# Optimization experiments

Hardware: AMD Instinct MI355X
Metric: run time of the kernel (lower is better)

The kernel has to match this reference:

```python
import jax, jax.numpy as jnp
import numpy as np

HEAD_DIM = 64

def setup_inputs() -> dict:
    key = jax.random.key(0)
    k1, k2, k3, k4 = jax.random.split(key, 4)
    B, S, D, H = 8, 2048, 1024, HEAD_DIM
    x = jax.random.normal(k1, (B, S, D), dtype=jnp.float32)
    scale = 1.0 / np.sqrt(D)
    W_q = jax.random.normal(k2, (H, D), dtype=jnp.float32) * scale
    W_k = jax.random.normal(k3, (H, D), dtype=jnp.float32) * scale
    W_v = jax.random.normal(k4, (H, D), dtype=jnp.float32) * scale
    return {"input_embeddings": x, "W_q": W_q, "W_k": W_k, "W_v": W_v}

def reference(input_embeddings, W_q, W_k, W_v):
    # Linear(model_dim, head_dim, bias=False): y = x @ W.T
    q = jnp.einsum('bsd,hd->bsh', input_embeddings, W_q)
    k = jnp.einsum('bsd,hd->bsh', input_embeddings, W_k)
    v = jnp.einsum('bsd,hd->bsh', input_embeddings, W_v)
    scores = jnp.einsum('bqh,bkh->bqk', q, k) / jnp.sqrt(jnp.float32(HEAD_DIM))
    S = scores.shape[-1]
    causal = jnp.tril(jnp.ones((S, S), dtype=bool))  # [S,S]
    scores = jnp.where(causal, scores, -jnp.inf)
    attn = jax.nn.softmax(scores, axis=-1)
    # dropout p=0.0 (eval-equivalent): identity
    return jnp.einsum('bqk,bkh->bqh', attn, v)
```

## Files before the change

### kernel.cpp

```cpp
#include <hip/hip_runtime.h>
#include <hip/hip_bf16.h>

typedef __bf16 bf16x8 __attribute__((ext_vector_type(8)));
typedef __bf16 bf16x4 __attribute__((ext_vector_type(4)));
typedef float  f32x4  __attribute__((ext_vector_type(4)));

#define NB  8
#define SEQ 2048
#define DM  1024
#define HD  64

#define WAITV4 asm volatile("s_waitcnt vmcnt(4)" ::: "memory")
#define WAITV0 asm volatile("s_waitcnt vmcnt(0)" ::: "memory")

__device__ __forceinline__ void gll16(const void* g, void* l) {
    __builtin_amdgcn_global_load_lds(
        (const __attribute__((address_space(1))) unsigned int*)g,
        (__attribute__((address_space(3))) unsigned int*)l, 16, 0, 0);
}

__global__ void k_convw(const float* __restrict__ Wq, const float* __restrict__ Wk,
                        const float* __restrict__ Wv, __bf16* __restrict__ Wb) {
    int idx = blockIdx.x * blockDim.x + threadIdx.x;
    int e = idx * 4;
    const float* src;
    if (e < 65536)       src = Wq + e;
    else if (e < 131072) src = Wk + (e - 65536);
    else                 src = Wv + (e - 131072);
    float4 v = *reinterpret_cast<const float4*>(src);
    bf16x4 o;
    o[0] = (__bf16)v.x; o[1] = (__bf16)v.y; o[2] = (__bf16)v.z; o[3] = (__bf16)v.w;
    *reinterpret_cast<bf16x4*>(Wb + e) = o;
}

__launch_bounds__(512, 4)
__global__ void k_proj(const float* __restrict__ X, const __bf16* __restrict__ Wb,
                       __bf16* __restrict__ Qb, __bf16* __restrict__ Kb,
                       __bf16* __restrict__ Vt) {
    __shared__ __align__(16) float  Xs[2][2048];
    __shared__ __align__(16) __bf16 Ws[2][12288];
    const int tid = threadIdx.x;
    const int w = tid >> 6, l = tid & 63;
    const int lr = l & 15, lg = l >> 4;
    const int wm = w >> 2, wn = w & 3;
    const int m0 = blockIdx.x * 32;

    const float* xsrc;
    {
        int u = w * 64 + l;
        int r_ = u >> 4, c_ = u & 15;
        xsrc = X + (size_t)(m0 + r_) * DM + (c_ ^ (r_ & 15)) * 4;
    }
    const __bf16* wsrc[3];
    #pragma unroll
    for (int j = 0; j < 3; ++j) {
        int u = w * 192 + j * 64 + l;
        int r_ = u >> 3, c_ = u & 7;
        wsrc[j] = Wb + (size_t)r_ * DM + (c_ ^ (r_ & 7)) * 8;
    }

    f32x4 acc[3];
    #pragma unroll
    for (int ct = 0; ct < 3; ++ct) acc[ct] = f32x4{0.f, 0.f, 0.f, 0.f};

    const int abase = (wm * 16 + lr) * 64;
    int bbase[3];
    #pragma unroll
    for (int ct = 0; ct < 3; ++ct) bbase[ct] = ((wn * 3 + ct) * 16 + lr) * 64;

    gll16(xsrc, &Xs[0][w * 256]);
    #pragma unroll
    for (int j = 0; j < 3; ++j) gll16(wsrc[j], &Ws[0][w * 1536 + j * 512]);

    #pragma unroll
    for (int t = 0; t < 16; ++t) {
        const int cur = t & 1;
        __builtin_amdgcn_s_barrier();
        if (t + 1 < 16) {
            gll16(xsrc + (size_t)(t + 1) * 64, &Xs[cur ^ 1][w * 256]);
            #pragma unroll
            for (int j = 0; j < 3; ++j)
                gll16(wsrc[j] + (size_t)(t + 1) * 64, &Ws[cur ^ 1][w * 1536 + j * 512]);
            WAITV4;
        } else {
            WAITV0;
        }
        const float*  Xp = &Xs[cur][0];
        const __bf16* Wp = &Ws[cur][0];
        #pragma unroll
        for (int ks = 0; ks < 2; ++ks) {
            f32x4 a0 = *reinterpret_cast<const f32x4*>(Xp + abase + ((ks * 8 + lg * 2)     ^ lr) * 4);
            f32x4 a1 = *reinterpret_cast<const f32x4*>(Xp + abase + ((ks * 8 + lg * 2 + 1) ^ lr) * 4);
            bf16x8 af;
            #pragma unroll
            for (int j = 0; j < 4; ++j) { af[j] = (__bf16)a0[j]; af[4 + j] = (__bf16)a1[j]; }
            #pragma unroll
            for (int ct = 0; ct < 3; ++ct) {
                bf16x8 bf = *reinterpret_cast<const bf16x8*>(
                    Wp + bbase[ct] + (((ks * 4 + lg) ^ (lr & 7)) * 8));
                acc[ct] = __builtin_amdgcn_mfma_f32_16x16x32_bf16(af, bf, acc[ct], 0, 0, 0);
            }
        }
    }

    const int rowbase = m0 + wm * 16 + lg * 4;
    #pragma unroll
    for (int ct = 0; ct < 3; ++ct) {
        const int ntile = wn * 3 + ct;
        const int mtx = ntile >> 2;
        const int d = (ntile & 3) * 16 + lr;
        if (mtx == 0) {
            #pragma unroll
            for (int r = 0; r < 4; ++r)
                Qb[(size_t)(rowbase + r) * HD + d] = (__bf16)(acc[ct][r] * 0.18033688f);
        } else if (mtx == 1) {
            #pragma unroll
            for (int r = 0; r < 4; ++r)
                Kb[(size_t)(rowbase + r) * HD + d] = (__bf16)acc[ct][r];
        } else {
            int bb = rowbase >> 11;
            int s0 = rowbase & 2047;
            bf16x4 vv;
            #pragma unroll
            for (int r = 0; r < 4; ++r) vv[r] = (__bf16)acc[ct][r];
            *reinterpret_cast<bf16x4*>(Vt + ((size_t)bb * HD + d) * SEQ + s0) = vv;
        }
    }
}

__launch_bounds__(512)
__global__ void k_attn(const __bf16* __restrict__ Qb, const __bf16* __restrict__ Kb,
                       const __bf16* __restrict__ Vt, __bf16* __restrict__ Opart,
                       float* __restrict__ ML, int T, int NC) {
    const int bid = blockIdx.x;
    const int b = bid / (16 * NC);
    const int rem = bid - b * 16 * NC;
    const int qt2 = rem / NC;
    const int c = rem - qt2 * NC;
    const int kmax = 2 * qt2 + 1;
    if (c * T > kmax) return;
    const int kt0 = c * T;
    const int nt = min(T, kmax + 1 - kt0);
    const int q0 = qt2 * 128;

    __shared__ __align__(16) __bf16 Ks[2][4096];
    __shared__ __align__(16) __bf16 Vs[2][4096];
    __shared__ __align__(16) __bf16 Ps[128][72];
    const int tid = threadIdx.x;
    const int w = tid >> 6, l = tid & 63;
    const int lr = l & 15, lg = l >> 4;
    const __bf16* Qp = Qb + (size_t)b * SEQ * HD;
    const __bf16* Kp = Kb + (size_t)b * SEQ * HD;
    const __bf16* Vp = Vt + (size_t)b * HD * SEQ;

    const int srow = tid >> 3;
    const int ssw  = ((l & 7) ^ (srow & 7)) * 8;
    const __bf16* ksrc = Kp + (size_t)(kt0 * 64 + srow) * HD + ssw;
    const __bf16* vsrc = Vp + (size_t)srow * SEQ + kt0 * 64 + ssw;
    const int myq = q0 + 16 * w + lr;

    bf16x8 qa[2];
    #pragma unroll
    for (int ks = 0; ks < 2; ++ks)
        qa[ks] = *reinterpret_cast<const bf16x8*>(
            Qp + (size_t)myq * HD + ks * 32 + lg * 8);

    f32x4 oacc[4];
    #pragma unroll
    for (int r = 0; r < 4; ++r) oacc[r] = f32x4{0.f, 0.f, 0.f, 0.f};
    float m = -1e30f, lsum = 0.f;

    gll16(ksrc, &Ks[0][w * 512]);
    gll16(vsrc, &Vs[0][w * 512]);

    for (int it = 0; it < nt; ++it) {
        const int kt = kt0 + it;
        const int k0 = kt * 64;
        const int cur = it & 1;
        __builtin_amdgcn_s_barrier();
        if (it + 1 < nt) {
            gll16(ksrc + (size_t)(it + 1) * 64 * HD, &Ks[cur ^ 1][w * 512]);
            gll16(vsrc + (it + 1) * 64,              &Vs[cur ^ 1][w * 512]);
            asm volatile("s_waitcnt vmcnt(2)" ::: "memory");
        } else {
            asm volatile("s_waitcnt vmcnt(0)" ::: "memory");
        }

        if (k0 > q0 + 16 * w + 15) continue;

        f32x4 sacc[4];
        #pragma unroll
        for (int t = 0; t < 4; ++t) sacc[t] = f32x4{0.f, 0.f, 0.f, 0.f};
        #pragma unroll
        for (int ks = 0; ks < 2; ++ks) {
            #pragma unroll
            for (int t = 0; t < 4; ++t) {
                bf16x8 kf = *reinterpret_cast<const bf16x8*>(
                    &Ks[cur][(16 * t + lr) * 64 + (((ks * 4 + lg) ^ (lr & 7)) * 8)]);
                sacc[t] = __builtin_amdgcn_mfma_f32_16x16x32_bf16(kf, qa[ks], sacc[t], 0, 0, 0);
            }
        }

        float pmax = -1e30f;
        if (k0 + 63 > q0 + 16 * w) {
            #pragma unroll
            for (int t = 0; t < 4; ++t)
                #pragma unroll
                for (int r = 0; r < 4; ++r) {
                    float v = sacc[t][r];
                    if ((k0 + 16 * t + lg * 4 + r) > myq) v = -1e30f;
                    sacc[t][r] = v;
                    pmax = fmaxf(pmax, v);
                }
        } else {
            #pragma unroll
            for (int t = 0; t < 4; ++t)
                #pragma unroll
                for (int r = 0; r < 4; ++r) pmax = fmaxf(pmax, sacc[t][r]);
        }
        pmax = fmaxf(pmax, __shfl_xor(pmax, 16));
        pmax = fmaxf(pmax, __shfl_xor(pmax, 32));

        if (!__all(pmax <= m + 12.f)) {
            float mnew = fmaxf(m, pmax);
            float fsc = exp2f(m - mnew);
            m = mnew;
            lsum *= fsc;
            #pragma unroll
            for (int r = 0; r < 4; ++r) {
                float fq = __shfl(fsc, (l & 48) + lg * 4 + r);
                #pragma unroll
                for (int t2 = 0; t2 < 4; ++t2) oacc[t2][r] *= fq;
            }
        }

        float rs = 0.f;
        #pragma unroll
        for (int t = 0; t < 4; ++t)
            #pragma unroll
            for (int r = 0; r < 4; ++r) {
                float p = exp2f(sacc[t][r] - m);
                sacc[t][r] = p;
                rs += p;
            }
        rs += __shfl_xor(rs, 16);
        rs += __shfl_xor(rs, 32);
        lsum += rs;

        #pragma unroll
        for (int t = 0; t < 4; ++t) {
            bf16x4 pv;
            #pragma unroll
            for (int r = 0; r < 4; ++r) pv[r] = (__bf16)sacc[t][r];
            *reinterpret_cast<bf16x4*>(&Ps[16 * w + lr][16 * t + lg * 4]) = pv;
        }

        #pragma unroll
        for (int ks = 0; ks < 2; ++ks) {
            bf16x8 pa = *reinterpret_cast<const bf16x8*>(&Ps[16 * w + lr][ks * 32 + lg * 8]);
            #pragma unroll
            for (int t2 = 0; t2 < 4; ++t2) {
                bf16x8 vb = *reinterpret_cast<const bf16x8*>(
                    &Vs[cur][(16 * t2 + lr) * 64 + (((ks * 4 + lg) ^ (lr & 7)) * 8)]);
                oacc[t2] = __builtin_amdgcn_mfma_f32_16x16x32_bf16(pa, vb, oacc[t2], 0, 0, 0);
            }
        }
    }

    const size_t slot = (size_t)bid;
    __bf16* op = Opart + slot * 8192;
    #pragma unroll
    for (int t2 = 0; t2 < 4; ++t2)
        #pragma unroll
        for (int r = 0; r < 4; ++r)
            op[(16 * w + lg * 4 + r) * 64 + 16 * t2 + lr] = (__bf16)oacc[t2][r];
    if (lg == 0) {
        float* ml = ML + slot * 256;
        int row = 16 * w + lr;
        ml[row * 2]     = m;
        ml[row * 2 + 1] = lsum;
    }
}

__launch_bounds__(512)
__global__ void k_merge(const __bf16* __restrict__ Opart, const float* __restrict__ ML,
                        float* __restrict__ Out, int T, int NC) {
    const int bq2 = blockIdx.x >> 1;
    const int half = blockIdx.x & 1;
    const int qt2 = bq2 & 15;
    const int nc = (2 * qt2 + 1) / T + 1;
    const int tid = threadIdx.x;
    const int row = tid >> 2;
    const int cg = (tid & 3) * 8 + half * 32;
    const int base = bq2 * NC;

    float M = -1e30f;
    for (int c = 0; c < nc; ++c)
        M = fmaxf(M, ML[(size_t)(base + c) * 256 + row * 2]);

    float L = 0.f;
    f32x4 a0{0,0,0,0}, a1{0,0,0,0};
    for (int c = 0; c < nc; ++c) {
        const float* ml = ML + (size_t)(base + c) * 256 + row * 2;
        float wgt = exp2f(ml[0] - M);
        L += ml[1] * wgt;
        bf16x8 v = *reinterpret_cast<const bf16x8*>(
            Opart + (size_t)(base + c) * 8192 + row * 64 + cg);
        #pragma unroll
        for (int j = 0; j < 4; ++j) {
            a0[j] += wgt * (float)v[j];
            a1[j] += wgt * (float)v[4 + j];
        }
    }
    float inv = 1.f / L;
    #pragma unroll
    for (int j = 0; j < 4; ++j) { a0[j] *= inv; a1[j] *= inv; }
    float* o = Out + ((size_t)bq2 * 128 + row) * 64 + cg;
    *reinterpret_cast<f32x4*>(o)     = a0;
    *reinterpret_cast<f32x4*>(o + 4) = a1;
}

extern "C" void kernel_launch(void* const* d_in, const int* in_sizes, int n_in,
                              void* d_out, int out_size, void* d_ws, size_t ws_size,
                              hipStream_t stream) {
    const float* x  = (const float*)d_in[0];
    const float* wq = (const float*)d_in[1];
    const float* wk = (const float*)d_in[2];
    const float* wv = (const float*)d_in[3];
    char* ws = (char*)d_ws;
    __bf16* Wb = (__bf16*)ws;
    __bf16* Qb = (__bf16*)(ws + 524288);
    __bf16* Kb = (__bf16*)(ws + 524288 + 2097152);
    __bf16* Vt = (__bf16*)(ws + 524288 + 2 * 2097152);
    const size_t base = 524288 + 3 * 2097152;
    float* out = (float*)d_out;

    int NC = (ws_size >= base + (size_t)(8 * 16 * 4) * 17408) ? 4 : 2;
    int T = 32 / NC;
    const int slots = 8 * 16 * NC;
    float*  ML    = (float*)(ws + base);
    __bf16* Opart = (__bf16*)(ws + base + (size_t)slots * 1024);

    hipLaunchKernelGGL(k_convw, dim3(192), dim3(256), 0, stream, wq, wk, wv, Wb);
    hipLaunchKernelGGL(k_proj,  dim3(512), dim3(512), 0, stream, x, Wb, Qb, Kb, Vt);
    hipLaunchKernelGGL(k_attn,  dim3(8 * 16 * NC), dim3(512), 0, stream,
                       Qb, Kb, Vt, Opart, ML, T, NC);
    hipLaunchKernelGGL(k_merge, dim3(256), dim3(512), 0, stream, Opart, ML, out, T, NC);
}
```

Baseline: 51.62 us.

## Process two 16-row query tiles per wave in attention, halve block size

Each wave in the attention kernel now handles 32 query rows (two 16-row MFMA tiles) instead of 16, and the block shrinks from 512 to 256 threads with launch bounds of 3 blocks per CU. Each K/V fragment read from LDS is reused for two MFMAs, which halves LDS traffic per unit of compute. Each thread now issues two async global-to-LDS loads per matrix per tile. The cost is roughly doubled accumulator and score registers per thread, plus coarser causal skipping because a wave covers 32 rows.

```diff
diff --git a/kernel.cpp b/kernel.cpp
--- a/kernel.cpp
+++ b/kernel.cpp
@@ -128,7 +128,7 @@
     }
 }
 
-__launch_bounds__(512)
+__launch_bounds__(256, 3)
 __global__ void k_attn(const __bf16* __restrict__ Qb, const __bf16* __restrict__ Kb,
                        const __bf16* __restrict__ Vt, __bf16* __restrict__ Opart,
                        float* __restrict__ ML, int T, int NC) {
@@ -153,25 +153,38 @@
     const __bf16* Kp = Kb + (size_t)b * SEQ * HD;
     const __bf16* Vp = Vt + (size_t)b * HD * SEQ;
 
-    const int srow = tid >> 3;
-    const int ssw  = ((l & 7) ^ (srow & 7)) * 8;
-    const __bf16* ksrc = Kp + (size_t)(kt0 * 64 + srow) * HD + ssw;
-    const __bf16* vsrc = Vp + (size_t)srow * SEQ + kt0 * 64 + ssw;
-    const int myq = q0 + 16 * w + lr;
-
-    bf16x8 qa[2];
-    #pragma unroll
-    for (int ks = 0; ks < 2; ++ks)
-        qa[ks] = *reinterpret_cast<const bf16x8*>(
-            Qp + (size_t)myq * HD + ks * 32 + lg * 8);
-
-    f32x4 oacc[4];
-    #pragma unroll
-    for (int r = 0; r < 4; ++r) oacc[r] = f32x4{0.f, 0.f, 0.f, 0.f};
-    float m = -1e30f, lsum = 0.f;
-
-    gll16(ksrc, &Ks[0][w * 512]);
-    gll16(vsrc, &Vs[0][w * 512]);
+    const __bf16* ksrc[2];
+    const __bf16* vsrc[2];
+    #pragma unroll
+    for (int j = 0; j < 2; ++j) {
+        int u = j * 256 + w * 64 + l;
+        int r_ = u >> 3, c_ = u & 7;
+        ksrc[j] = Kp + (size_t)(kt0 * 64 + r_) * HD + ((c_ ^ (r_ & 7)) * 8);
+        vsrc[j] = Vp + (size_t)r_ * SEQ + kt0 * 64 + ((c_ ^ (r_ & 7)) * 8);
+    }
+    const int myq0 = q0 + 32 * w + lr;
+    const int myq1 = myq0 + 16;
+
+    bf16x8 qa0[2], qa1[2];
+    #pragma unroll
+    for (int ks = 0; ks < 2; ++ks) {
+        qa0[ks] = *reinterpret_cast<const bf16x8*>(Qp + (size_t)myq0 * HD + ks * 32 + lg * 8);
+        qa1[ks] = *reinterpret_cast<const bf16x8*>(Qp + (size_t)myq1 * HD + ks * 32 + lg * 8);
+    }
+
+    f32x4 oacc0[4], oacc1[4];
+    #pragma unroll
+    for (int r = 0; r < 4; ++r) {
+        oacc0[r] = f32x4{0.f, 0.f, 0.f, 0.f};
+        oacc1[r] = f32x4{0.f, 0.f, 0.f, 0.f};
+    }
+    float m0v = -1e30f, l0v = 0.f, m1v = -1e30f, l1v = 0.f;
+
+    #pragma unroll
+    for (int j = 0; j < 2; ++j) {
+        gll16(ksrc[j], &Ks[0][(j * 256 + w * 64) * 8]);
+        gll16(vsrc[j], &Vs[0][(j * 256 + w * 64) * 8]);
+    }
 
     for (int it = 0; it < nt; ++it) {
         const int kt = kt0 + it;
@@ -179,90 +192,147 @@
         const int cur = it & 1;
         __builtin_amdgcn_s_barrier();
         if (it + 1 < nt) {
-            gll16(ksrc + (size_t)(it + 1) * 64 * HD, &Ks[cur ^ 1][w * 512]);
-            gll16(vsrc + (it + 1) * 64,              &Vs[cur ^ 1][w * 512]);
-            asm volatile("s_waitcnt vmcnt(2)" ::: "memory");
+            #pragma unroll
+            for (int j = 0; j < 2; ++j) {
+                gll16(ksrc[j] + (size_t)(it + 1) * 64 * HD, &Ks[cur ^ 1][(j * 256 + w * 64) * 8]);
+                gll16(vsrc[j] + (it + 1) * 64,              &Vs[cur ^ 1][(j * 256 + w * 64) * 8]);
+            }
+            WAITV4;
         } else {
-            asm volatile("s_waitcnt vmcnt(0)" ::: "memory");
-        }
-
-        if (k0 > q0 + 16 * w + 15) continue;
-
-        f32x4 sacc[4];
-        #pragma unroll
-        for (int t = 0; t < 4; ++t) sacc[t] = f32x4{0.f, 0.f, 0.f, 0.f};
+            WAITV0;
+        }
+
+        if (k0 > q0 + 32 * w + 31) continue;
+
+        f32x4 s0[4], s1[4];
+        #pragma unroll
+        for (int t = 0; t < 4; ++t) { s0[t] = f32x4{0,0,0,0}; s1[t] = f32x4{0,0,0,0}; }
         #pragma unroll
         for (int ks = 0; ks < 2; ++ks) {
             #pragma unroll
             for (int t = 0; t < 4; ++t) {
                 bf16x8 kf = *reinterpret_cast<const bf16x8*>(
                     &Ks[cur][(16 * t + lr) * 64 + (((ks * 4 + lg) ^ (lr & 7)) * 8)]);
-                sacc[t] = __builtin_amdgcn_mfma_f32_16x16x32_bf16(kf, qa[ks], sacc[t], 0, 0, 0);
-            }
-        }
-
-        float pmax = -1e30f;
-        if (k0 + 63 > q0 + 16 * w) {
+                s0[t] = __builtin_amdgcn_mfma_f32_16x16x32_bf16(kf, qa0[ks], s0[t], 0, 0, 0);
+                s1[t] = __builtin_amdgcn_mfma_f32_16x16x32_bf16(kf, qa1[ks], s1[t], 0, 0, 0);
+            }
+        }
+
+        {
+            float pmax = -1e30f;
+            if (k0 + 63 > myq0 - lr) {
+                #pragma unroll
+                for (int t = 0; t < 4; ++t)
+                    #pragma unroll
+                    for (int r = 0; r < 4; ++r) {
+                        float v = s0[t][r];
+                        if ((k0 + 16 * t + lg * 4 + r) > myq0) v = -1e30f;
+                        s0[t][r] = v;
+                        pmax = fmaxf(pmax, v);
+                    }
+            } else {
+                #pragma unroll
+                for (int t = 0; t < 4; ++t)
+                    #pragma unroll
+                    for (int r = 0; r < 4; ++r) pmax = fmaxf(pmax, s0[t][r]);
+            }
+            pmax = fmaxf(pmax, __shfl_xor(pmax, 16));
+            pmax = fmaxf(pmax, __shfl_xor(pmax, 32));
+            if (!__all(pmax <= m0v + 12.f)) {
+                float mnew = fmaxf(m0v, pmax);
+                float fsc = exp2f(m0v - mnew);
+                m0v = mnew;
+                l0v *= fsc;
+                #pragma unroll
+                for (int r = 0; r < 4; ++r) {
+                    float fq = __shfl(fsc, (l & 48) + lg * 4 + r);
+                    #pragma unroll
+                    for (int t2 = 0; t2 < 4; ++t2) oacc0[t2][r] *= fq;
+                }
+            }
+            float rs = 0.f;
             #pragma unroll
             for (int t = 0; t < 4; ++t)
                 #pragma unroll
                 for (int r = 0; r < 4; ++r) {
-                    float v = sacc[t][r];
-                    if ((k0 + 16 * t + lg * 4 + r) > myq) v = -1e30f;
-                    sacc[t][r] = v;
-                    pmax = fmaxf(pmax, v);
+                    float p = exp2f(s0[t][r] - m0v);
+                    s0[t][r] = p;
+                    rs += p;
                 }
-        } else {
+            rs += __shfl_xor(rs, 16);
+            rs += __shfl_xor(rs, 32);
+            l0v += rs;
+            #pragma unroll
+            for (int t = 0; t < 4; ++t) {
+                bf16x4 pv;
+                #pragma unroll
+                for (int r = 0; r < 4; ++r) pv[r] = (__bf16)s0[t][r];
+                *reinterpret_cast<bf16x4*>(&Ps[32 * w + lr][16 * t + lg * 4]) = pv;
+            }
+        }
+        {
+            float pmax = -1e30f;
+            if (k0 + 63 > myq1 - lr) {
+                #pragma unroll
+                for (int t = 0; t < 4; ++t)
+                    #pragma unroll
+                    for (int r = 0; r < 4; ++r) {
+                        float v = s1[t][r];
+                        if ((k0 + 16 * t + lg * 4 + r) > myq1) v = -1e30f;
+                        s1[t][r] = v;
+                        pmax = fmaxf(pmax, v);
+                    }
+            } else {
+                #pragma unroll
+                for (int t = 0; t < 4; ++t)
+                    #pragma unroll
+                    for (int r = 0; r < 4; ++r) pmax = fmaxf(pmax, s1[t][r]);
+            }
+            pmax = fmaxf(pmax, __shfl_xor(pmax, 16));
+            pmax = fmaxf(pmax, __shfl_xor(pmax, 32));
+            if (!__all(pmax <= m1v + 12.f)) {
+                float mnew = fmaxf(m1v, pmax);
+                float fsc = exp2f(m1v - mnew);
+                m1v = mnew;
+                l1v *= fsc;
+                #pragma unroll
+                for (int r = 0; r < 4; ++r) {
+                    float fq = __shfl(fsc, (l & 48) + lg * 4 + r);
+                    #pragma unroll
+                    for (int t2 = 0; t2 < 4; ++t2) oacc1[t2][r] *= fq;
+                }
+            }
+            float rs = 0.f;
             #pragma unroll
             for (int t = 0; t < 4; ++t)
                 #pragma unroll
-                for (int r = 0; r < 4; ++r) pmax = fmaxf(pmax, sacc[t][r]);
-        }
-        pmax = fmaxf(pmax, __shfl_xor(pmax, 16));
-        pmax = fmaxf(pmax, __shfl_xor(pmax, 32));
-
-        if (!__all(pmax <= m + 12.f)) {
-            float mnew = fmaxf(m, pmax);
-            float fsc = exp2f(m - mnew);
-            m = mnew;
-            lsum *= fsc;
-            #pragma unroll
-            for (int r = 0; r < 4; ++r) {
-                float fq = __shfl(fsc, (l & 48) + lg * 4 + r);
-                #pragma unroll
-                for (int t2 = 0; t2 < 4; ++t2) oacc[t2][r] *= fq;
-            }
-        }
-
-        float rs = 0.f;
-        #pragma unroll
-        for (int t = 0; t < 4; ++t)
-            #pragma unroll
-            for (int r = 0; r < 4; ++r) {
-                float p = exp2f(sacc[t][r] - m);
-                sacc[t][r] = p;
-                rs += p;
-            }
-        rs += __shfl_xor(rs, 16);
-        rs += __shfl_xor(rs, 32);
-        lsum += rs;
-
-        #pragma unroll
-        for (int t = 0; t < 4; ++t) {
-            bf16x4 pv;
-            #pragma unroll
-            for (int r = 0; r < 4; ++r) pv[r] = (__bf16)sacc[t][r];
-            *reinterpret_cast<bf16x4*>(&Ps[16 * w + lr][16 * t + lg * 4]) = pv;
+                for (int r = 0; r < 4; ++r) {
+                    float p = exp2f(s1[t][r] - m1v);
+                    s1[t][r] = p;
+                    rs += p;
+                }
+            rs += __shfl_xor(rs, 16);
+            rs += __shfl_xor(rs, 32);
+            l1v += rs;
+            #pragma unroll
+            for (int t = 0; t < 4; ++t) {
+                bf16x4 pv;
+                #pragma unroll
+                for (int r = 0; r < 4; ++r) pv[r] = (__bf16)s1[t][r];
+                *reinterpret_cast<bf16x4*>(&Ps[32 * w + 16 + lr][16 * t + lg * 4]) = pv;
+            }
         }
 
         #pragma unroll
         for (int ks = 0; ks < 2; ++ks) {
-            bf16x8 pa = *reinterpret_cast<const bf16x8*>(&Ps[16 * w + lr][ks * 32 + lg * 8]);
+            bf16x8 pa0 = *reinterpret_cast<const bf16x8*>(&Ps[32 * w + lr][ks * 32 + lg * 8]);
+            bf16x8 pa1 = *reinterpret_cast<const bf16x8*>(&Ps[32 * w + 16 + lr][ks * 32 + lg * 8]);
             #pragma unroll
             for (int t2 = 0; t2 < 4; ++t2) {
                 bf16x8 vb = *reinterpret_cast<const bf16x8*>(
                     &Vs[cur][(16 * t2 + lr) * 64 + (((ks * 4 + lg) ^ (lr & 7)) * 8)]);
-                oacc[t2] = __builtin_amdgcn_mfma_f32_16x16x32_bf16(pa, vb, oacc[t2], 0, 0, 0);
+                oacc0[t2] = __builtin_amdgcn_mfma_f32_16x16x32_bf16(pa0, vb, oacc0[t2], 0, 0, 0);
+                oacc1[t2] = __builtin_amdgcn_mfma_f32_16x16x32_bf16(pa1, vb, oacc1[t2], 0, 0, 0);
             }
         }
     }
@@ -272,13 +342,17 @@
     #pragma unroll
     for (int t2 = 0; t2 < 4; ++t2)
         #pragma unroll
-        for (int r = 0; r < 4; ++r)
-            op[(16 * w + lg * 4 + r) * 64 + 16 * t2 + lr] = (__bf16)oacc[t2][r];
+        for (int r = 0; r < 4; ++r) {
+            op[(32 * w + lg * 4 + r) * 64 + 16 * t2 + lr]      = (__bf16)oacc0[t2][r];
+            op[(32 * w + 16 + lg * 4 + r) * 64 + 16 * t2 + lr] = (__bf16)oacc1[t2][r];
+        }
     if (lg == 0) {
         float* ml = ML + slot * 256;
-        int row = 16 * w + lr;
-        ml[row * 2]     = m;
-        ml[row * 2 + 1] = lsum;
+        int row0 = 32 * w + lr;
+        ml[row0 * 2]            = m0v;
+        ml[row0 * 2 + 1]        = l0v;
+        ml[(row0 + 16) * 2]     = m1v;
+        ml[(row0 + 16) * 2 + 1] = l1v;
     }
 }
 
@@ -343,7 +417,7 @@
 
     hipLaunchKernelGGL(k_convw, dim3(192), dim3(256), 0, stream, wq, wk, wv, Wb);
     hipLaunchKernelGGL(k_proj,  dim3(512), dim3(512), 0, stream, x, Wb, Qb, Kb, Vt);
-    hipLaunchKernelGGL(k_attn,  dim3(8 * 16 * NC), dim3(512), 0, stream,
+    hipLaunchKernelGGL(k_attn,  dim3(8 * 16 * NC), dim3(256), 0, stream,
                        Qb, Kb, Vt, Opart, ML, T, NC);
     hipLaunchKernelGGL(k_merge, dim3(256), dim3(512), 0, stream, Opart, ML, out, T, NC);
 }
```

Result: slower. 54.25 us (+5.1%).
